# Performance work log

Hardware: AMD Instinct MI355X
Metric: run time of the kernel (lower is better)

The kernel has to match this reference:

```python
import jax, jax.numpy as jnp
import numpy as np

N = 50000      # nodes
E = 600000     # edges
A = 8          # max attrs per node
DT = 64        # node type embed dim
DA = 64        # node attr embed dim
C = DT + DA    # annotation dim = GGNN channels
T = 16         # num node types
TE = 4         # num edge types
L = 4          # num_agg_steps
B = 256        # num graphs
VATTR = 1000   # num node attrs
ENC = 128      # encoder_output_dim
NCLS = 10      # decoder output classes


def setup_inputs() -> dict:
    key = jax.random.key(0)
    ks = jax.random.split(key, 16)
    s = 0.05
    x_type = jax.random.randint(ks[0], (N,), 0, T)
    x_attrs = jax.random.randint(ks[1], (N, A), 0, VATTR)
    x_attrs_mask = jax.random.randint(ks[2], (N,), 1, A + 1)  # >=1 valid attr per node
    edge_index = jax.random.randint(ks[3], (2, E), 0, N)
    edge_attr = jax.random.randint(ks[4], (E,), 0, TE)
    batch = jnp.sort(jax.random.randint(ks[5], (N,), 0, B))
    return {
        'x_type': x_type, 'x_attrs': x_attrs, 'x_attrs_mask': x_attrs_mask,
        'edge_index': edge_index, 'edge_attr': edge_attr,
        'num_graphs': int(B), 'batch': batch,
        'type_emb': jax.random.normal(ks[6], (T, DT)) * s,
        'attr_emb': jax.random.normal(ks[7], (VATTR, DA)) * s,
        'W_msg': jax.random.normal(ks[8], (L, TE, C, C)) * s,
        'W_ih': jax.random.normal(ks[9], (3 * C, C)) * s,
        'W_hh': jax.random.normal(ks[10], (3 * C, C)) * s,
        'b_ih': jnp.zeros((3 * C,)),
        'b_hh': jnp.zeros((3 * C,)),
        'w_attn': jax.random.normal(ks[11], (C,)) * s,
        'b_attn': jnp.zeros(()),
        'W_enc': jax.random.normal(ks[12], (T * C, ENC)) * s,
        'b_enc': jnp.zeros((ENC,)),
        'W_dec': jax.random.normal(ks[13], (ENC, NCLS)) * s,
        'b_dec': jnp.zeros((NCLS,)),
    }


def _gru_cell(m, h, W_ih, W_hh, b_ih, b_hh):
    gi = m @ W_ih.T + b_ih            # [N, 3C]
    gh = h @ W_hh.T + b_hh            # [N, 3C]
    ir, iz, inn = jnp.split(gi, 3, axis=-1)
    hr, hz, hn = jnp.split(gh, 3, axis=-1)
    r = jax.nn.sigmoid(ir + hr)
    z = jax.nn.sigmoid(iz + hz)
    n = jnp.tanh(inn + r * hn)
    return (1.0 - z) * n + z * h


def reference(x_type, x_attrs, x_attrs_mask, edge_index, edge_attr, num_graphs, batch,
              type_emb, attr_emb, W_msg, W_ih, W_hh, b_ih, b_hh,
              w_attn, b_attn, W_enc, b_enc, W_dec, b_dec):
    n = x_type.shape[0]
    # --- embed node types and ragged-mean attribute embeddings ---
    t_emb = type_emb[x_type]                                   # [N, DT]
    a_all = attr_emb[x_attrs]                                  # [N, A, DA]
    valid = (jnp.arange(A)[None, :] < x_attrs_mask[:, None]).astype(a_all.dtype)
    a_emb = (a_all * valid[..., None]).sum(1) / jnp.maximum(x_attrs_mask, 1)[:, None].astype(a_all.dtype)
    x = jnp.concatenate([t_emb, a_emb], axis=1)                # [N, C]

    # --- GatedGraphConv with per-edge-type weights (sum aggregation + GRU) ---
    src, dst = edge_index[0], edge_index[1]
    for l in range(L):
        h_all = jnp.einsum('nc,tcd->tnd', x, W_msg[l])         # [TE, N, C]
        m_e = h_all.reshape(TE * n, C)[edge_attr * n + src]    # [E, C] gather per edge
        m = jax.ops.segment_sum(m_e, dst, num_segments=n)      # [N, C]
        x = _gru_cell(m, x, W_ih, W_hh, b_ih, b_hh)

    # --- per-(graph, node_type) segment mean (zeros for empty groups) ---
    seg = batch * T + x_type                                   # [N]
    S = num_graphs * T
    sums = jax.ops.segment_sum(x, seg, num_segments=S)         # [B*T, C]
    cnt = jax.ops.segment_sum(jnp.ones((n,), x.dtype), seg, num_segments=S)
    agg = jnp.where(cnt[:, None] > 0, sums / jnp.maximum(cnt, 1.0)[:, None], 0.0)
    agg = agg.reshape(num_graphs, T, C)                        # [B, T, C]

    # --- attention over node types, flatten, encode, decode ---
    w = agg @ w_attn + b_attn                                  # [B, T]
    attn = jax.nn.softmax(w, axis=-1)
    flat = (attn[..., None] * agg).reshape(num_graphs, T * C)  # [B, T*C]
    enc = flat @ W_enc + b_enc                                 # [B, ENC]
    return enc @ W_dec + b_dec                                 # [B, NCLS]
```

## Files before the change

### kernel.cpp

```cpp
#include <hip/hip_runtime.h>
#include <hip/hip_bf16.h>

#define NN 50000
#define EE 600000
#define AA 8
#define CC 128
#define TT 16
#define TE 4
#define LL 4
#define BB 256
#define ENC 128
#define NCLS 10

typedef __attribute__((ext_vector_type(8))) short bf16x8;
typedef __attribute__((ext_vector_type(4))) float fx4;

__device__ __forceinline__ float b2f(ushort u) {
    union { float f; uint32_t i; } v; v.i = ((uint32_t)u) << 16; return v.f;
}
__device__ __forceinline__ ushort f2b(float f) {
    union { float f; uint32_t i; } v; v.f = f;
    uint32_t x = v.i;
    x += 0x7FFFu + ((x >> 16) & 1u);
    return (ushort)(x >> 16);
}
__device__ __forceinline__ float ldw(const void* p, long i, int isf) {
    return isf ? ((const float*)p)[i] : b2f(((const ushort*)p)[i]);
}
__device__ __forceinline__ float sigm(float t) { return 1.f / (1.f + __expf(-t)); }

__global__ void sniff_kernel(int* flag, const void* W_enc_raw) {
    const ushort* u = (const ushort*)W_enc_raw;
    int good = 0;
    for (int i = 0; i < 256; ++i) {
        ushort v = u[i];
        int ex = (v >> 7) & 0xFF;
        if (v == 0 || (ex >= 100 && ex <= 126)) ++good;
    }
    *flag = (good >= 230) ? 0 : 1;
}

__global__ __launch_bounds__(256) void wmsgT_kernel(ushort* __restrict__ wT,
                                                    const void* __restrict__ W,
                                                    const int* __restrict__ flag) {
    const int isf = *flag;
    int idx = blockIdx.x * 256 + threadIdx.x;
    int lt = idx >> 14, rem = idx & 16383, d = rem >> 7, c = rem & 127;
    long src = ((long)lt << 14) + c * 128 + d;
    wT[idx] = isf ? f2b(((const float*)W)[src]) : ((const ushort*)W)[src];
}

__global__ __launch_bounds__(256) void wgru_kernel(ushort* __restrict__ wgb,
                                                   const void* __restrict__ Wih,
                                                   const void* __restrict__ Whh,
                                                   const int* __restrict__ flag) {
    const int isf = *flag;
    int idx = blockIdx.x * 256 + threadIdx.x;
    if (idx >= 98304) return;
    int ih = (idx < 49152);
    int off = ih ? idx : idx - 49152;
    wgb[idx] = f2b(ldw(ih ? Wih : Whh, off, isf));
}

__global__ __launch_bounds__(256) void wencT_kernel(ushort* __restrict__ wencT,
                                                    const void* __restrict__ W_enc,
                                                    const int* __restrict__ flag) {
    const int isf = *flag;
    int idx = blockIdx.x * 256 + threadIdx.x;
    int j = idx >> 11, k = idx & 2047;
    wencT[idx] = f2b(ldw(W_enc, (long)k * ENC + j, isf));
}

__global__ __launch_bounds__(256) void bconv_kernel(float* __restrict__ cvt,
                                                    const void* __restrict__ bih, const void* __restrict__ bhh,
                                                    const void* __restrict__ b_enc, const void* __restrict__ w_attn,
                                                    const void* __restrict__ b_dec, const void* __restrict__ b_attn,
                                                    const void* __restrict__ W_dec,
                                                    const int* __restrict__ flag) {
    const int isf = *flag;
    int i = blockIdx.x * 256 + threadIdx.x;
    if (i < 384) cvt[i] = ldw(bih, i, isf);
    else if (i < 768) cvt[i] = ldw(bhh, i - 384, isf);
    else if (i < 896) cvt[i] = ldw(b_enc, i - 768, isf);
    else if (i < 1024) cvt[i] = ldw(w_attn, i - 896, isf);
    else if (i < 1034) cvt[i] = ldw(b_dec, i - 1024, isf);
    else if (i == 1034) cvt[i] = ldw(b_attn, 0, isf);
    else if (i >= 1040 && i < 2320) cvt[i] = ldw(W_dec, i - 1040, isf);
}

__global__ __launch_bounds__(256) void embed_kernel(
    float* __restrict__ x, ushort* __restrict__ xbf,
    const int* __restrict__ x_type, const int* __restrict__ x_attrs,
    const int* __restrict__ x_mask, const void* __restrict__ type_emb,
    const void* __restrict__ attr_emb, const int* __restrict__ flag) {
    const int isf = *flag;
    int idx = blockIdx.x * 256 + threadIdx.x;
    int n = idx >> 6, c = idx & 63;
    if (n >= NN) return;
    int ty = x_type[n];
    float tv = ldw(type_emb, ty * 64 + c, isf);
    x[n * CC + c] = tv;
    xbf[n * CC + c] = f2b(tv);
    int cnt = x_mask[n];
    float s = 0.f;
    for (int a = 0; a < cnt; ++a) s += ldw(attr_emb, x_attrs[n * AA + a] * 64 + c, isf);
    float av = s / (float)cnt;
    x[n * CC + 64 + c] = av;
    xbf[n * CC + 64 + c] = f2b(av);
}

__global__ __launch_bounds__(256) void deg_kernel(int* __restrict__ cnt, const int* __restrict__ ei) {
    int e = blockIdx.x * 256 + threadIdx.x;
    if (e < EE) atomicAdd(&cnt[ei[EE + e]], 1);
}
__global__ __launch_bounds__(256) void scan1_kernel(int* __restrict__ cnt, int* __restrict__ btot) {
    __shared__ int s[256];
    int tid = threadIdx.x, i = blockIdx.x * 256 + tid;
    int v = (i < NN) ? cnt[i] : 0;
    s[tid] = v; __syncthreads();
    for (int off = 1; off < 256; off <<= 1) {
        int t = (tid >= off) ? s[tid - off] : 0; __syncthreads();
        s[tid] += t; __syncthreads();
    }
    if (i < NN) cnt[i] = s[tid] - v;
    if (tid == 255) btot[blockIdx.x] = s[255];
}
__global__ __launch_bounds__(256) void scan2_kernel(int* __restrict__ btot, int nb) {
    __shared__ int s[256];
    int tid = threadIdx.x;
    int v = (tid < nb) ? btot[tid] : 0;
    s[tid] = v; __syncthreads();
    for (int off = 1; off < 256; off <<= 1) {
        int t = (tid >= off) ? s[tid - off] : 0; __syncthreads();
        s[tid] += t; __syncthreads();
    }
    if (tid < nb) btot[tid] = s[tid] - v;
}
__global__ __launch_bounds__(256) void scan3_kernel(int* __restrict__ cnt, const int* __restrict__ btot) {
    int i = blockIdx.x * 256 + threadIdx.x;
    if (i < NN) cnt[i] += btot[blockIdx.x];
}
__global__ __launch_bounds__(256) void fill_kernel(uint* __restrict__ csr, int* __restrict__ cnt,
                                                   const int* __restrict__ ei, const int* __restrict__ ea) {
    int e = blockIdx.x * 256 + threadIdx.x;
    if (e >= EE) return;
    int d = ei[EE + e];
    int pos = atomicAdd(&cnt[d], 1);
    csr[pos] = (uint)ei[e] | ((uint)ea[e] << 16);
}

__global__ __launch_bounds__(256) void msg_mfma4(
    ushort* __restrict__ h4, const ushort* __restrict__ xbf, const ushort* __restrict__ wT) {
    int tid = threadIdx.x;
    int t = tid >> 6, l = tid & 63;
    int node0 = blockIdx.x * 32;
    int lr = l & 15, lk = (l >> 4) * 8;
    bf16x8 af[2][4];
#pragma unroll
    for (int rt = 0; rt < 2; ++rt)
#pragma unroll
        for (int ks = 0; ks < 4; ++ks)
            af[rt][ks] = *(const bf16x8*)&xbf[(size_t)(node0 + rt * 16 + lr) * CC + ks * 32 + lk];
#pragma unroll
    for (int ct = 0; ct < 8; ++ct) {
        bf16x8 bfr[4];
#pragma unroll
        for (int ks = 0; ks < 4; ++ks)
            bfr[ks] = *(const bf16x8*)&wT[(size_t)(t * 128 + ct * 16 + lr) * 128 + ks * 32 + lk];
        fx4 acc0 = {0.f, 0.f, 0.f, 0.f}, acc1 = {0.f, 0.f, 0.f, 0.f};
#pragma unroll
        for (int ks = 0; ks < 4; ++ks) {
            acc0 = __builtin_amdgcn_mfma_f32_16x16x32_bf16(af[0][ks], bfr[ks], acc0, 0, 0, 0);
            acc1 = __builtin_amdgcn_mfma_f32_16x16x32_bf16(af[1][ks], bfr[ks], acc1, 0, 0, 0);
        }
#pragma unroll
        for (int r = 0; r < 4; ++r) {
            int n0 = node0 + (l >> 4) * 4 + r;
            int n1 = n0 + 16;
            if (n0 < NN) h4[((size_t)t * NN + n0) * CC + ct * 16 + lr] = f2b(acc0[r]);
            if (n1 < NN) h4[((size_t)t * NN + n1) * CC + ct * 16 + lr] = f2b(acc1[r]);
        }
    }
}

__global__ __launch_bounds__(256) void gather_kernel(
    ushort* __restrict__ mbf, const ushort* __restrict__ h4,
    const uint* __restrict__ csr, const int* __restrict__ endp) {
    int w = threadIdx.x >> 6, l = threadIdx.x & 63;
    int node = blockIdx.x * 4 + w;
    int start = (node == 0) ? 0 : endp[node - 1];
    int end = endp[node];
    int c0 = l * 2;
    float s0 = 0.f, s1 = 0.f;
    for (int i = start; i < end; ++i) {
        uint pk = csr[i];
        uint src = pk & 0xFFFFu, t = pk >> 16;
        uint hv = *(const uint*)&h4[(((size_t)t * NN + src) << 7) + c0];
        s0 += b2f((ushort)(hv & 0xFFFFu));
        s1 += b2f((ushort)(hv >> 16));
    }
    *(uint*)&mbf[((size_t)node << 7) + c0] = (uint)f2b(s0) | ((uint)f2b(s1) << 16);
}

__global__ __launch_bounds__(256) void gru_mfma(
    float* __restrict__ x, ushort* __restrict__ xbf, const ushort* __restrict__ mbf,
    const ushort* __restrict__ wgb, const float* __restrict__ cvt) {
    int tid = threadIdx.x;
    int w = tid >> 6, l = tid & 63;
    int node0 = blockIdx.x * 32;
    int lr = l & 15, lk = (l >> 4) * 8;
    bf16x8 mf[2][4], xf[2][4];
#pragma unroll
    for (int rt = 0; rt < 2; ++rt)
#pragma unroll
        for (int ks = 0; ks < 4; ++ks) {
            size_t ro = (size_t)(node0 + rt * 16 + lr) * CC + ks * 32 + lk;
            mf[rt][ks] = *(const bf16x8*)&mbf[ro];
            xf[rt][ks] = *(const bf16x8*)&xbf[ro];
        }
    __syncthreads();
#pragma unroll
    for (int cc = 0; cc < 2; ++cc) {
        int ct = w * 2 + cc;
        int row0 = ct * 16 + lr;
        fx4 ai[3][2], ah[3][2];
#pragma unroll
        for (int s = 0; s < 3; ++s)
#pragma unroll
            for (int rt = 0; rt < 2; ++rt) { ai[s][rt] = (fx4){0,0,0,0}; ah[s][rt] = (fx4){0,0,0,0}; }
#pragma unroll
        for (int ks = 0; ks < 4; ++ks) {
            int ko = ks * 32 + lk;
            bf16x8 bI[3], bH[3];
#pragma unroll
            for (int s = 0; s < 3; ++s) {
                bI[s] = *(const bf16x8*)&wgb[(size_t)(s * 128 + row0) * 128 + ko];
                bH[s] = *(const bf16x8*)&wgb[49152 + (size_t)(s * 128 + row0) * 128 + ko];
            }
#pragma unroll
            for (int s = 0; s < 3; ++s)
#pragma unroll
                for (int rt = 0; rt < 2; ++rt) {
                    ai[s][rt] = __builtin_amdgcn_mfma_f32_16x16x32_bf16(mf[rt][ks], bI[s], ai[s][rt], 0, 0, 0);
                    ah[s][rt] = __builtin_amdgcn_mfma_f32_16x16x32_bf16(xf[rt][ks], bH[s], ah[s][rt], 0, 0, 0);
                }
        }
        float bi0 = cvt[row0],        bh0 = cvt[384 + row0];
        float bi1 = cvt[128 + row0],  bh1 = cvt[512 + row0];
        float bi2 = cvt[256 + row0],  bh2 = cvt[640 + row0];
#pragma unroll
        for (int rt = 0; rt < 2; ++rt)
#pragma unroll
            for (int r = 0; r < 4; ++r) {
                int node = node0 + rt * 16 + (l >> 4) * 4 + r;
                if (node >= NN) continue;
                float rg = sigm(ai[0][rt][r] + bi0 + ah[0][rt][r] + bh0);
                float zg = sigm(ai[1][rt][r] + bi1 + ah[1][rt][r] + bh1);
                float ny = ai[2][rt][r] + bi2 + rg * (ah[2][rt][r] + bh2);
                float ng = 2.f * sigm(2.f * ny) - 1.f;
                size_t xi = (size_t)node * CC + row0;
                float xo = x[xi];
                float xn = (1.f - zg) * ng + zg * xo;
                x[xi] = xn;
                xbf[xi] = f2b(xn);
            }
    }
}

__global__ __launch_bounds__(256) void agg_kernel(
    float* __restrict__ sums, float* __restrict__ cnt, const float* __restrict__ x,
    const int* __restrict__ batch, const int* __restrict__ x_type) {
    int idx = blockIdx.x * 256 + threadIdx.x;
    int n = idx >> 7, c = idx & 127;
    int seg = batch[n] * TT + x_type[n];
    atomicAdd(&sums[seg * CC + c], x[idx]);
    if (c == 0) atomicAdd(&cnt[seg], 1.0f);
}

__global__ __launch_bounds__(256) void attnflat_kernel(
    ushort* __restrict__ flatbf, const float* __restrict__ sums, const float* __restrict__ cnt,
    const float* __restrict__ cvt) {
    __shared__ float agg_s[TT][CC + 1];
    __shared__ float wpart[TT][8];
    __shared__ float attn_s[TT];
    int b = blockIdx.x, tid = threadIdx.x;
#pragma unroll
    for (int q = 0; q < 8; ++q) {
        int idx = tid + q * 256;
        int t = idx >> 7, c = idx & 127;
        float cv = cnt[b * TT + t];
        agg_s[t][c] = cv > 0.f ? sums[(size_t)(b * TT + t) * CC + c] / cv : 0.f;
    }
    __syncthreads();
    if (tid < 128) {
        int t = tid >> 3, p = tid & 7;
        float acc = 0.f;
        for (int i = 0; i < 16; ++i) acc += agg_s[t][p * 16 + i] * cvt[896 + p * 16 + i];
        wpart[t][p] = acc;
    }
    __syncthreads();
    if (tid < 16) {
        float acc = cvt[1034];
        for (int p = 0; p < 8; ++p) acc += wpart[tid][p];
        attn_s[tid] = acc;
    }
    __syncthreads();
    if (tid == 0) {
        float mx = attn_s[0];
        for (int t = 1; t < TT; ++t) mx = fmaxf(mx, attn_s[t]);
        float ssum = 0.f, ex[TT];
        for (int t = 0; t < TT; ++t) { ex[t] = __expf(attn_s[t] - mx); ssum += ex[t]; }
        for (int t = 0; t < TT; ++t) attn_s[t] = ex[t] / ssum;
    }
    __syncthreads();
#pragma unroll
    for (int q = 0; q < 8; ++q) {
        int idx = tid + q * 256;
        int t = idx >> 7, c = idx & 127;
        flatbf[(size_t)b * 2048 + idx] = f2b(agg_s[t][c] * attn_s[t]);
    }
}

__global__ __launch_bounds__(256) void enc_mfma(
    float* __restrict__ encp, const ushort* __restrict__ flatbf, const ushort* __restrict__ wencT) {
    int tid = threadIdx.x;
    int w = tid >> 6, l = tid & 63;
    int bid = blockIdx.x;
    int m0 = (bid >> 2) * 16;
    int kc = (bid & 3) * 512;
    int lr = l & 15, lk = (l >> 4) * 8;
    fx4 acc0 = {0,0,0,0}, acc1 = {0,0,0,0};
    int ct0 = w * 2, ct1 = w * 2 + 1;
#pragma unroll
    for (int ks = 0; ks < 16; ++ks) {
        int ko = kc + ks * 32 + lk;
        bf16x8 af = *(const bf16x8*)&flatbf[(size_t)(m0 + lr) * 2048 + ko];
        bf16x8 b0 = *(const bf16x8*)&wencT[(size_t)(ct0 * 16 + lr) * 2048 + ko];
        bf16x8 b1 = *(const bf16x8*)&wencT[(size_t)(ct1 * 16 + lr) * 2048 + ko];
        acc0 = __builtin_amdgcn_mfma_f32_16x16x32_bf16(af, b0, acc0, 0, 0, 0);
        acc1 = __builtin_amdgcn_mfma_f32_16x16x32_bf16(af, b1, acc1, 0, 0, 0);
    }
#pragma unroll
    for (int r = 0; r < 4; ++r) {
        int row = m0 + (l >> 4) * 4 + r;
        encp[(size_t)(bid & 3) * BB * ENC + (size_t)row * ENC + ct0 * 16 + lr] = acc0[r];
        encp[(size_t)(bid & 3) * BB * ENC + (size_t)row * ENC + ct1 * 16 + lr] = acc1[r];
    }
}

__global__ __launch_bounds__(256) void dec_kernel(
    void* __restrict__ out, const float* __restrict__ encp, const float* __restrict__ cvt,
    const int* __restrict__ flag) {
    const int isf = *flag;
    __shared__ float encs[ENC];
    int b = blockIdx.x, tid = threadIdx.x;
    if (tid < 128) {
        float e = cvt[768 + tid];
#pragma unroll
        for (int p = 0; p < 4; ++p) e += encp[(size_t)p * BB * ENC + (size_t)b * ENC + tid];
        encs[tid] = e;
    }
    __syncthreads();
    if (tid < NCLS) {
        float acc = cvt[1024 + tid];
        for (int j = 0; j < ENC; ++j) acc += encs[j] * cvt[1040 + j * NCLS + tid];
        int oi = b * NCLS + tid;
        if (isf) ((float*)out)[oi] = acc;
        else ((ushort*)out)[oi] = f2b(acc);
    }
}

extern "C" void kernel_launch(void* const* d_in, const int* in_sizes, int n_in,
                              void* d_out, int out_size, void* d_ws, size_t ws_size,
                              hipStream_t stream) {
    const int* x_type      = (const int*)d_in[0];
    const int* x_attrs     = (const int*)d_in[1];
    const int* x_mask      = (const int*)d_in[2];
    const int* edge_index  = (const int*)d_in[3];
    const int* edge_attr   = (const int*)d_in[4];
    const int* batch       = (const int*)d_in[6];
    const void* type_emb   = d_in[7];
    const void* attr_emb   = d_in[8];
    const void* W_msg      = d_in[9];
    const void* W_ih       = d_in[10];
    const void* W_hh       = d_in[11];
    const void* b_ih       = d_in[12];
    const void* b_hh       = d_in[13];
    const void* w_attn     = d_in[14];
    const void* b_attn     = d_in[15];
    const void* W_enc      = d_in[16];
    const void* b_enc      = d_in[17];
    const void* W_dec      = d_in[18];
    const void* b_dec      = d_in[19];

    char* p = (char*)d_ws;
    float*  x     = (float*)p;           p += (size_t)NN * CC * 4;
    ushort* xbf   = (ushort*)p;          p += (size_t)NN * CC * 2;
    ushort* mbf   = (ushort*)p;          p += (size_t)NN * CC * 2;
    ushort* h4    = (ushort*)p;          p += (size_t)4 * NN * CC * 2;
    ushort* wT    = (ushort*)p;          p += (size_t)16 * 128 * 128 * 2;
    ushort* wgb   = (ushort*)p;          p += (size_t)2 * 384 * 128 * 2;
    ushort* wencT = (ushort*)p;          p += (size_t)ENC * 2048 * 2;
    ushort* flatbf= (ushort*)p;          p += (size_t)BB * 2048 * 2;
    float*  encp  = (float*)p;           p += (size_t)4 * BB * ENC * 4;
    float*  cvt   = (float*)p;           p += 2320 * 4;
    float*  sums  = (float*)p;           p += (size_t)BB * TT * CC * 4;
    float*  cnta  = (float*)p;           p += (size_t)BB * TT * 4;
    uint*   csr   = (uint*)p;            p += (size_t)EE * 4;
    int*    cptr  = (int*)p;             p += (size_t)NN * 4;
    int*    btot  = (int*)p;             p += 256 * 4;
    int*    flag  = (int*)p;

    sniff_kernel<<<1, 1, 0, stream>>>(flag, W_enc);
    wmsgT_kernel<<<1024, 256, 0, stream>>>(wT, W_msg, flag);
    wgru_kernel<<<384, 256, 0, stream>>>(wgb, W_ih, W_hh, flag);
    wencT_kernel<<<1024, 256, 0, stream>>>(wencT, W_enc, flag);
    bconv_kernel<<<10, 256, 0, stream>>>(cvt, b_ih, b_hh, b_enc, w_attn, b_dec, b_attn, W_dec, flag);
    embed_kernel<<<(NN * 64) / 256, 256, 0, stream>>>(x, xbf, x_type, x_attrs, x_mask,
                                                      type_emb, attr_emb, flag);

    const int NB = (NN + 255) / 256;
    hipMemsetAsync(cptr, 0, (size_t)NN * sizeof(int), stream);
    deg_kernel<<<(EE + 255) / 256, 256, 0, stream>>>(cptr, edge_index);
    scan1_kernel<<<NB, 256, 0, stream>>>(cptr, btot);
    scan2_kernel<<<1, 256, 0, stream>>>(btot, NB);
    scan3_kernel<<<NB, 256, 0, stream>>>(cptr, btot);
    fill_kernel<<<(EE + 255) / 256, 256, 0, stream>>>(csr, cptr, edge_index, edge_attr);

    const int tile_grid = (NN + 31) / 32;
    for (int l = 0; l < LL; ++l) {
        msg_mfma4<<<tile_grid, 256, 0, stream>>>(h4, xbf, wT + (size_t)l * 4 * 128 * 128);
        gather_kernel<<<NN / 4, 256, 0, stream>>>(mbf, h4, csr, cptr);
        gru_mfma<<<tile_grid, 256, 0, stream>>>(x, xbf, mbf, wgb, cvt);
    }

    hipMemsetAsync(sums, 0, (size_t)(BB * TT * CC + BB * TT) * sizeof(float), stream);
    agg_kernel<<<(NN * CC) / 256, 256, 0, stream>>>(sums, cnta, x, batch, x_type);
    attnflat_kernel<<<BB, 256, 0, stream>>>(flatbf, sums, cnta, cvt);
    enc_mfma<<<64, 256, 0, stream>>>(encp, flatbf, wencT);
    dec_kernel<<<BB, 256, 0, stream>>>(d_out, encp, cvt, flag);
}
```

Before: 850.4 us.

## Drop fp32 state, fuse segment aggregation into last GRU, stage message stores via LDS

Removes the fp32 copy of the node state and keeps only the bf16 copy, so the GRU reads its previous state from bf16 and skips an fp32 read and write per element. The per-(graph, type) sum aggregation is fused into the final GRU launch through atomics, which removes the separate agg kernel and its re-read of x. The message GEMM now stages its output tile in shared memory and writes it out as coalesced 16-byte stores instead of scattered 2-byte stores. The cost is lower precision in the recurrent state, which now round-trips through bf16 every step.

```diff
diff --git a/kernel.cpp b/kernel.cpp
--- a/kernel.cpp
+++ b/kernel.cpp
@@ -14,6 +14,7 @@
 
 typedef __attribute__((ext_vector_type(8))) short bf16x8;
 typedef __attribute__((ext_vector_type(4))) float fx4;
+typedef __attribute__((ext_vector_type(4))) uint ux4;
 
 __device__ __forceinline__ float b2f(ushort u) {
     union { float f; uint32_t i; } v; v.i = ((uint32_t)u) << 16; return v.f;
@@ -89,7 +90,7 @@
 }
 
 __global__ __launch_bounds__(256) void embed_kernel(
-    float* __restrict__ x, ushort* __restrict__ xbf,
+    ushort* __restrict__ xbf,
     const int* __restrict__ x_type, const int* __restrict__ x_attrs,
     const int* __restrict__ x_mask, const void* __restrict__ type_emb,
     const void* __restrict__ attr_emb, const int* __restrict__ flag) {
@@ -98,15 +99,11 @@
     int n = idx >> 6, c = idx & 63;
     if (n >= NN) return;
     int ty = x_type[n];
-    float tv = ldw(type_emb, ty * 64 + c, isf);
-    x[n * CC + c] = tv;
-    xbf[n * CC + c] = f2b(tv);
+    xbf[n * CC + c] = f2b(ldw(type_emb, ty * 64 + c, isf));
     int cnt = x_mask[n];
     float s = 0.f;
     for (int a = 0; a < cnt; ++a) s += ldw(attr_emb, x_attrs[n * AA + a] * 64 + c, isf);
-    float av = s / (float)cnt;
-    x[n * CC + 64 + c] = av;
-    xbf[n * CC + 64 + c] = f2b(av);
+    xbf[n * CC + 64 + c] = f2b(s / (float)cnt);
 }
 
 __global__ __launch_bounds__(256) void deg_kernel(int* __restrict__ cnt, const int* __restrict__ ei) {
@@ -151,6 +148,7 @@
 
 __global__ __launch_bounds__(256) void msg_mfma4(
     ushort* __restrict__ h4, const ushort* __restrict__ xbf, const ushort* __restrict__ wT) {
+    __shared__ ushort h_s[4][32][128];
     int tid = threadIdx.x;
     int t = tid >> 6, l = tid & 63;
     int node0 = blockIdx.x * 32;
@@ -175,10 +173,21 @@
         }
 #pragma unroll
         for (int r = 0; r < 4; ++r) {
-            int n0 = node0 + (l >> 4) * 4 + r;
-            int n1 = n0 + 16;
-            if (n0 < NN) h4[((size_t)t * NN + n0) * CC + ct * 16 + lr] = f2b(acc0[r]);
-            if (n1 < NN) h4[((size_t)t * NN + n1) * CC + ct * 16 + lr] = f2b(acc1[r]);
+            int nl = (l >> 4) * 4 + r;
+            h_s[t][nl][ct * 16 + lr]      = f2b(acc0[r]);
+            h_s[t][nl + 16][ct * 16 + lr] = f2b(acc1[r]);
+        }
+    }
+    __syncthreads();
+    const uint* ls = (const uint*)&h_s[0][0][0];
+#pragma unroll
+    for (int q = 0; q < 8; ++q) {
+        int i4 = q * 256 + tid;
+        int t2 = i4 >> 9, rem = i4 & 511;
+        int node = rem >> 4, chunk = rem & 15;
+        if (node0 + node < NN) {
+            ux4 v = *(const ux4*)&ls[i4 * 4];
+            *(ux4*)&h4[((size_t)t2 * NN + node0 + node) * CC + chunk * 8] = v;
         }
     }
 }
@@ -202,9 +211,12 @@
     *(uint*)&mbf[((size_t)node << 7) + c0] = (uint)f2b(s0) | ((uint)f2b(s1) << 16);
 }
 
+template <int AGG>
 __global__ __launch_bounds__(256) void gru_mfma(
-    float* __restrict__ x, ushort* __restrict__ xbf, const ushort* __restrict__ mbf,
-    const ushort* __restrict__ wgb, const float* __restrict__ cvt) {
+    ushort* __restrict__ xbf, const ushort* __restrict__ mbf,
+    const ushort* __restrict__ wgb, const float* __restrict__ cvt,
+    float* __restrict__ sums, float* __restrict__ cnta,
+    const int* __restrict__ batch, const int* __restrict__ x_type) {
     int tid = threadIdx.x;
     int w = tid >> 6, l = tid & 63;
     int node0 = blockIdx.x * 32;
@@ -259,22 +271,16 @@
                 float ny = ai[2][rt][r] + bi2 + rg * (ah[2][rt][r] + bh2);
                 float ng = 2.f * sigm(2.f * ny) - 1.f;
                 size_t xi = (size_t)node * CC + row0;
-                float xo = x[xi];
+                float xo = b2f(xbf[xi]);
                 float xn = (1.f - zg) * ng + zg * xo;
-                x[xi] = xn;
                 xbf[xi] = f2b(xn);
+                if (AGG) {
+                    int seg = batch[node] * TT + x_type[node];
+                    atomicAdd(&sums[(size_t)seg * CC + row0], xn);
+                    if (row0 == 0) atomicAdd(&cnta[seg], 1.0f);
+                }
             }
     }
-}
-
-__global__ __launch_bounds__(256) void agg_kernel(
-    float* __restrict__ sums, float* __restrict__ cnt, const float* __restrict__ x,
-    const int* __restrict__ batch, const int* __restrict__ x_type) {
-    int idx = blockIdx.x * 256 + threadIdx.x;
-    int n = idx >> 7, c = idx & 127;
-    int seg = batch[n] * TT + x_type[n];
-    atomicAdd(&sums[seg * CC + c], x[idx]);
-    if (c == 0) atomicAdd(&cnt[seg], 1.0f);
 }
 
 __global__ __launch_bounds__(256) void attnflat_kernel(
@@ -394,7 +400,6 @@
     const void* b_dec      = d_in[19];
 
     char* p = (char*)d_ws;
-    float*  x     = (float*)p;           p += (size_t)NN * CC * 4;
     ushort* xbf   = (ushort*)p;          p += (size_t)NN * CC * 2;
     ushort* mbf   = (ushort*)p;          p += (size_t)NN * CC * 2;
     ushort* h4    = (ushort*)p;          p += (size_t)4 * NN * CC * 2;
@@ -416,7 +421,7 @@
     wgru_kernel<<<384, 256, 0, stream>>>(wgb, W_ih, W_hh, flag);
     wencT_kernel<<<1024, 256, 0, stream>>>(wencT, W_enc, flag);
     bconv_kernel<<<10, 256, 0, stream>>>(cvt, b_ih, b_hh, b_enc, w_attn, b_dec, b_attn, W_dec, flag);
-    embed_kernel<<<(NN * 64) / 256, 256, 0, stream>>>(x, xbf, x_type, x_attrs, x_mask,
+    embed_kernel<<<(NN * 64) / 256, 256, 0, stream>>>(xbf, x_type, x_attrs, x_mask,
                                                       type_emb, attr_emb, flag);
 
     const int NB = (NN + 255) / 256;
@@ -427,15 +432,18 @@
     scan3_kernel<<<NB, 256, 0, stream>>>(cptr, btot);
     fill_kernel<<<(EE + 255) / 256, 256, 0, stream>>>(csr, cptr, edge_index, edge_attr);
 
+    hipMemsetAsync(sums, 0, (size_t)(BB * TT * CC + BB * TT) * sizeof(float), stream);
+
     const int tile_grid = (NN + 31) / 32;
     for (int l = 0; l < LL; ++l) {
         msg_mfma4<<<tile_grid, 256, 0, stream>>>(h4, xbf, wT + (size_t)l * 4 * 128 * 128);
         gather_kernel<<<NN / 4, 256, 0, stream>>>(mbf, h4, csr, cptr);
-        gru_mfma<<<tile_grid, 256, 0, stream>>>(x, xbf, mbf, wgb, cvt);
-    }
-
-    hipMemsetAsync(sums, 0, (size_t)(BB * TT * CC + BB * TT) * sizeof(float), stream);
-    agg_kernel<<<(NN * CC) / 256, 256, 0, stream>>>(sums, cnta, x, batch, x_type);
+        if (l < LL - 1)
+            gru_mfma<0><<<tile_grid, 256, 0, stream>>>(xbf, mbf, wgb, cvt, sums, cnta, batch, x_type);
+        else
+            gru_mfma<1><<<tile_grid, 256, 0, stream>>>(xbf, mbf, wgb, cvt, sums, cnta, batch, x_type);
+    }
+
     attnflat_kernel<<<BB, 256, 0, stream>>>(flatbf, sums, cnta, cvt);
     enc_mfma<<<64, 256, 0, stream>>>(encp, flatbf, wencT);
     dec_kernel<<<BB, 256, 0, stream>>>(d_out, encp, cvt, flag);
```

New measurement: 797.7 us. -6.2%, faster.
